# Kernel optimization log

Hardware: AMD Instinct MI355X
Metric: run time of the kernel (lower is better)

The kernel has to match this reference:

```python
import jax, jax.numpy as jnp
import numpy as np

NUM_HEADS = 16
KEY_DIM = 64
EPS = 1e-6


def setup_inputs() -> dict:
    key = jax.random.key(0)
    k0, k1, k2, k3, k4 = jax.random.split(key, 5)
    B, S, E = 4, 4096, NUM_HEADS * KEY_DIM
    scale = 1.0 / np.sqrt(KEY_DIM)
    return {
        "query": jax.random.normal(k0, (B, S, E), dtype=jnp.float32),
        "Wq": jax.random.normal(k1, (NUM_HEADS, KEY_DIM, KEY_DIM), dtype=jnp.float32) * scale,
        "Wk": jax.random.normal(k2, (NUM_HEADS, KEY_DIM, KEY_DIM), dtype=jnp.float32) * scale,
        "Wv": jax.random.normal(k3, (NUM_HEADS, KEY_DIM, KEY_DIM), dtype=jnp.float32) * scale,
        "Wo": jax.random.normal(k4, (E, E), dtype=jnp.float32) * (1.0 / np.sqrt(E)),
    }


def reference(query, Wq, Wk, Wv, Wo):
    # Self-attention: key = value = query (per call() defaults).
    B, S, E = query.shape
    H, D = NUM_HEADS, KEY_DIM
    # split_heads: (B, S, E) -> (B, H, S, D)
    x = jnp.transpose(query.reshape(B, S, H, D), (0, 2, 1, 3))
    # Per-head linear projections (all heads batched in one einsum each).
    q = jnp.einsum("bhsd,hde->bhse", x, Wq)
    k = jnp.einsum("bhsd,hde->bhse", x, Wk)
    v = jnp.einsum("bhsd,hde->bhse", x, Wv)
    # Kernel feature map phi(x) = elu(x) + 1 (strictly positive).
    phi_q = jax.nn.elu(q) + 1.0
    phi_k = jax.nn.elu(k) + 1.0
    # Linear (non-causal) attention: O(S*D^2) instead of O(S^2*D).
    kv = jnp.einsum("bhsd,bhse->bhde", phi_k, v)        # (B,H,D,D)
    k_sum = jnp.sum(phi_k, axis=2)                       # (B,H,D)
    z = jnp.einsum("bhsd,bhd->bhs", phi_q, k_sum)        # (B,H,S)
    ctx = jnp.einsum("bhsd,bhde->bhse", phi_q, kv) / (z[..., None] + EPS)
    # combine_heads: (B,H,S,D) -> (B,S,E), then output projection (no bias).
    combined = jnp.transpose(ctx, (0, 2, 1, 3)).reshape(B, S, H * D)
    return combined @ Wo
```

## Files before the change

### kernel.cpp

```cpp
#include <hip/hip_runtime.h>
#include <stdint.h>

#define S_LEN 4096
#define NHEADS 16
#define DHEAD 64
#define EMB 1024
#define NBATCH 4
#define NBH (NBATCH * NHEADS)

typedef unsigned short u16t;
typedef __attribute__((ext_vector_type(8))) short short8;
typedef __attribute__((ext_vector_type(4))) float f32x4;

__device__ __forceinline__ u16t f2bf(float f) {
  unsigned int x = __float_as_uint(f);
  x += 0x7fffu + ((x >> 16) & 1u);
  return (u16t)(x >> 16);
}
__device__ __forceinline__ unsigned int pack2(float a, float b) {
  return (unsigned int)f2bf(a) | ((unsigned int)f2bf(b) << 16);
}
__device__ __forceinline__ float bf2f(u16t u) { return __uint_as_float(((unsigned int)u) << 16); }
__device__ __forceinline__ float phifn(float v) { return v > 0.f ? v + 1.f : __expf(v); }

__device__ __forceinline__ void stage_x_bf16(const float* __restrict__ xg,
                                             u16t* __restrict__ xs, int t) {
#pragma unroll
  for (int i = 0; i < 8; ++i) {
    int fi = i * 256 + t;
    int r = fi >> 4, c4 = fi & 15;
    float4 v = *(const float4*)(xg + (size_t)r * EMB + c4 * 4);
    uint2 p;
    p.x = pack2(v.x, v.y);
    p.y = pack2(v.z, v.w);
    *(uint2*)(&xs[r * 72 + c4 * 4]) = p;
  }
}

__device__ __forceinline__ void stage_w8k(const u16t* __restrict__ wg,
                                          u16t* __restrict__ lds, int t) {
#pragma unroll
  for (int c = 0; c < 2; ++c) {
    const u16t* src = wg + (size_t)(c * 256 + t) * 8;
    char* dst = (char*)lds + c * 4096 + ((t >> 6) << 10);
    __builtin_amdgcn_global_load_lds((const __attribute__((address_space(1))) unsigned int*)src,
                                     (__attribute__((address_space(3))) unsigned int*)dst,
                                     16, 0, 0);
  }
}

__global__ __launch_bounds__(256) void la_prep(const float* __restrict__ Wq,
                                               const float* __restrict__ Wk,
                                               const float* __restrict__ Wv,
                                               u16t* __restrict__ WqT,
                                               u16t* __restrict__ WkT,
                                               u16t* __restrict__ WvT) {
  __shared__ float tmp[64][65];
  int blk = blockIdx.x;
  int mat = blk >> 4, h = blk & 15;
  const float* src = (mat == 0 ? Wq : (mat == 1 ? Wk : Wv)) + (size_t)h * 4096;
  u16t* dst = (mat == 0 ? WqT : (mat == 1 ? WkT : WvT)) + (size_t)h * 4096;
  int t = threadIdx.x;
#pragma unroll
  for (int p = 0; p < 16; ++p) {
    int i = p * 256 + t;
    tmp[i >> 6][i & 63] = src[i];
  }
  __syncthreads();
#pragma unroll
  for (int p = 0; p < 16; ++p) {
    int i = p * 256 + t;
    int e = i >> 6, r = i & 63, o = r >> 3, j = r & 7;
    dst[i] = f2bf(tmp[((o ^ (e & 7)) << 3) + j][e]);
  }
}

__global__ __launch_bounds__(256) void la_wot(const float* __restrict__ Wo,
                                              u16t* __restrict__ WoT) {
  __shared__ float t[64][65];
  int n0 = blockIdx.x * 64, k0 = blockIdx.y * 64;
  int tx = threadIdx.x, ty = threadIdx.y;
  for (int r = ty; r < 64; r += 4) t[r][tx] = Wo[(size_t)(k0 + r) * EMB + n0 + tx];
  __syncthreads();
  for (int r = ty; r < 64; r += 4)
    WoT[(size_t)(n0 + r) * EMB + k0 + tx] = f2bf(t[tx][r]);
}

__global__ __launch_bounds__(256) void la_kv2(const float* __restrict__ q,
                                              const u16t* __restrict__ WkT,
                                              const u16t* __restrict__ WvT,
                                              float* __restrict__ kvpart,
                                              float* __restrict__ kspart) {
  union Sm {
    struct { u16t xs[128 * 72]; u16t wk[4096]; u16t wv[4096]; } a;
    struct { u16t pkT[64 * 136]; u16t vT[64 * 136]; } b;
  };
  __shared__ Sm sm;
  int blk = blockIdx.x;
  int bh = blk >> 5, tile = blk & 31;
  int b = bh >> 4, h = bh & 15;
  int s0 = tile << 7;
  int t = threadIdx.x;
  int wave = t >> 6, lane = t & 63, l16 = lane & 15, g = lane >> 4;

  stage_x_bf16(q + ((size_t)b * S_LEN + s0) * EMB + h * 64, sm.a.xs, t);
  stage_w8k(WkT + (size_t)h * 4096, sm.a.wk, t);
  stage_w8k(WvT + (size_t)h * 4096, sm.a.wv, t);
  __syncthreads();

  f32x4 aK[2][4], aV[2][4];
#pragma unroll
  for (int m = 0; m < 2; ++m)
#pragma unroll
    for (int n = 0; n < 4; ++n) { aK[m][n] = 0.f; aV[m][n] = 0.f; }

  short8 af[2][2];
#pragma unroll
  for (int m = 0; m < 2; ++m)
#pragma unroll
    for (int kk = 0; kk < 2; ++kk)
      af[m][kk] = *(const short8*)(&sm.a.xs[(wave * 32 + m * 16 + l16) * 72 + kk * 32 + g * 8]);
#pragma unroll
  for (int n = 0; n < 4; ++n) {
    int e = n * 16 + l16;
#pragma unroll
    for (int kk = 0; kk < 2; ++kk) {
      int op = (kk * 4 + g) ^ (l16 & 7);
      short8 bK = *(const short8*)(&sm.a.wk[e * 64 + op * 8]);
      short8 bV = *(const short8*)(&sm.a.wv[e * 64 + op * 8]);
#pragma unroll
      for (int m = 0; m < 2; ++m) {
        aK[m][n] = __builtin_amdgcn_mfma_f32_16x16x32_bf16(af[m][kk], bK, aK[m][n], 0, 0, 0);
        aV[m][n] = __builtin_amdgcn_mfma_f32_16x16x32_bf16(af[m][kk], bV, aV[m][n], 0, 0, 0);
      }
    }
  }
  __syncthreads();

#pragma unroll
  for (int m = 0; m < 2; ++m)
#pragma unroll
    for (int n = 0; n < 4; ++n) {
      int e = n * 16 + l16;
#pragma unroll
      for (int j = 0; j < 4; ++j) {
        int s = wave * 32 + m * 16 + g * 4 + j;
        sm.b.pkT[e * 136 + s] = f2bf(phifn(aK[m][n][j]));
        sm.b.vT[e * 136 + s] = f2bf(aV[m][n][j]);
      }
    }
  __syncthreads();

  f32x4 kacc[4];
#pragma unroll
  for (int n = 0; n < 4; ++n) kacc[n] = 0.f;
#pragma unroll
  for (int ks = 0; ks < 4; ++ks) {
    short8 pa = *(const short8*)(&sm.b.pkT[(wave * 16 + l16) * 136 + ks * 32 + g * 8]);
#pragma unroll
    for (int n = 0; n < 4; ++n) {
      short8 vb = *(const short8*)(&sm.b.vT[(n * 16 + l16) * 136 + ks * 32 + g * 8]);
      kacc[n] = __builtin_amdgcn_mfma_f32_16x16x32_bf16(pa, vb, kacc[n], 0, 0, 0);
    }
  }
  float* kp = kvpart + (size_t)blk * 4096;
#pragma unroll
  for (int n = 0; n < 4; ++n)
#pragma unroll
    for (int j = 0; j < 4; ++j)
      kp[(wave * 16 + g * 4 + j) * 64 + n * 16 + l16] = kacc[n][j];

  if (t < 64) {
    float a = 0.f;
#pragma unroll 8
    for (int s = 0; s < 128; ++s) a += bf2f(sm.b.pkT[t * 136 + s]);
    kspart[(size_t)blk * 64 + t] = a;
  }
}

__global__ __launch_bounds__(256) void la_red2(const float* __restrict__ kvpart,
                                               const float* __restrict__ kspart,
                                               u16t* __restrict__ kvT_g,
                                               float* __restrict__ ksum_g) {
  __shared__ float kvs[64][65];
  int bh = blockIdx.x, t = threadIdx.x;
  float acc[16];
#pragma unroll
  for (int p = 0; p < 16; ++p) acc[p] = 0.f;
  for (int part = 0; part < 32; ++part) {
    const float* base = kvpart + ((size_t)bh * 32 + part) * 4096;
#pragma unroll
    for (int p = 0; p < 16; ++p) acc[p] += base[p * 256 + t];
  }
#pragma unroll
  for (int p = 0; p < 16; ++p) {
    int i = p * 256 + t;
    kvs[i >> 6][i & 63] = acc[p];
  }
  if (t < 64) {
    float a = 0.f;
    for (int part = 0; part < 32; ++part) a += kspart[((size_t)bh * 32 + part) * 64 + t];
    ksum_g[(size_t)bh * 64 + t] = a;
  }
  __syncthreads();
#pragma unroll
  for (int p = 0; p < 16; ++p) {
    int i = p * 256 + t;
    int e = i >> 6, r = i & 63, o = r >> 3, j = r & 7;
    kvT_g[(size_t)bh * 4096 + i] = f2bf(kvs[((o ^ (e & 7)) << 3) + j][e]);
  }
}

__global__ __launch_bounds__(256) void la_ctx2(const float* __restrict__ q,
                                               const u16t* __restrict__ WqT,
                                               const u16t* __restrict__ kvT_g,
                                               const float* __restrict__ ksum_g,
                                               u16t* __restrict__ comb) {
  __shared__ u16t xs[128 * 72];
  __shared__ u16t wq[4096];
  __shared__ u16t kvt[4096];
  __shared__ float ks[64];
  int blk = blockIdx.x;
  int bh = blk >> 5, tile = blk & 31;
  int b = bh >> 4, h = bh & 15;
  int s0 = tile << 7;
  int t = threadIdx.x;
  int wave = t >> 6, lane = t & 63, l16 = lane & 15, g = lane >> 4;

  stage_x_bf16(q + ((size_t)b * S_LEN + s0) * EMB + h * 64, xs, t);
  stage_w8k(WqT + (size_t)h * 4096, wq, t);
  stage_w8k(kvT_g + (size_t)bh * 4096, kvt, t);
  if (t < 64) ks[t] = ksum_g[(size_t)bh * 64 + t];
  __syncthreads();

  f32x4 aQ[2][4];
#pragma unroll
  for (int m = 0; m < 2; ++m)
#pragma unroll
    for (int n = 0; n < 4; ++n) aQ[m][n] = 0.f;
  short8 af[2][2];
#pragma unroll
  for (int m = 0; m < 2; ++m)
#pragma unroll
    for (int kk = 0; kk < 2; ++kk)
      af[m][kk] = *(const short8*)(&xs[(wave * 32 + m * 16 + l16) * 72 + kk * 32 + g * 8]);
#pragma unroll
  for (int n = 0; n < 4; ++n) {
    int e = n * 16 + l16;
#pragma unroll
    for (int kk = 0; kk < 2; ++kk) {
      int op = (kk * 4 + g) ^ (l16 & 7);
      short8 bQ = *(const short8*)(&wq[e * 64 + op * 8]);
#pragma unroll
      for (int m = 0; m < 2; ++m)
        aQ[m][n] = __builtin_amdgcn_mfma_f32_16x16x32_bf16(af[m][kk], bQ, aQ[m][n], 0, 0, 0);
    }
  }

  float ph[2][4][4];
#pragma unroll
  for (int m = 0; m < 2; ++m)
#pragma unroll
    for (int n = 0; n < 4; ++n)
#pragma unroll
      for (int j = 0; j < 4; ++j) ph[m][n][j] = phifn(aQ[m][n][j]);

  float z[2][4];
#pragma unroll
  for (int m = 0; m < 2; ++m)
#pragma unroll
    for (int j = 0; j < 4; ++j) {
      float zp = 0.f;
#pragma unroll
      for (int n = 0; n < 4; ++n) zp = fmaf(ph[m][n][j], ks[n * 16 + l16], zp);
      zp += __shfl_xor(zp, 1);
      zp += __shfl_xor(zp, 2);
      zp += __shfl_xor(zp, 4);
      zp += __shfl_xor(zp, 8);
      z[m][j] = zp;
    }
  __syncthreads();

#pragma unroll
  for (int m = 0; m < 2; ++m)
#pragma unroll
    for (int n = 0; n < 4; ++n)
#pragma unroll
      for (int j = 0; j < 4; ++j)
        xs[(wave * 32 + m * 16 + g * 4 + j) * 72 + n * 16 + l16] = f2bf(ph[m][n][j]);
  __syncthreads();

  f32x4 nacc[2][4];
#pragma unroll
  for (int m = 0; m < 2; ++m)
#pragma unroll
    for (int n = 0; n < 4; ++n) nacc[m][n] = 0.f;
#pragma unroll
  for (int kk = 0; kk < 2; ++kk) {
    short8 pa[2];
#pragma unroll
    for (int m = 0; m < 2; ++m)
      pa[m] = *(const short8*)(&xs[(wave * 32 + m * 16 + l16) * 72 + kk * 32 + g * 8]);
#pragma unroll
    for (int n = 0; n < 4; ++n) {
      int e = n * 16 + l16;
      int op = (kk * 4 + g) ^ (l16 & 7);
      short8 kb = *(const short8*)(&kvt[e * 64 + op * 8]);
#pragma unroll
      for (int m = 0; m < 2; ++m)
        nacc[m][n] = __builtin_amdgcn_mfma_f32_16x16x32_bf16(pa[m], kb, nacc[m][n], 0, 0, 0);
    }
  }
  __syncthreads();

#pragma unroll
  for (int m = 0; m < 2; ++m)
#pragma unroll
    for (int j = 0; j < 4; ++j) {
      float inv = 1.f / (z[m][j] + 1e-6f);
      int s = wave * 32 + m * 16 + g * 4 + j;
#pragma unroll
      for (int n = 0; n < 4; ++n)
        xs[s * 72 + n * 16 + l16] = f2bf(nacc[m][n][j] * inv);
    }
  __syncthreads();

#pragma unroll
  for (int i = 0; i < 4; ++i) {
    int c = i * 256 + t;
    int r = c >> 3, qd = c & 7;
    uint4 v = *(const uint4*)(&xs[r * 72 + qd * 8]);
    *(uint4*)(&comb[((size_t)b * S_LEN + s0 + r) * EMB + h * 64 + qd * 8]) = v;
  }
}

__device__ __forceinline__ void stage_half(const u16t* __restrict__ gbase,
                                           u16t* __restrict__ lbuf,
                                           int half, int t) {
#pragma unroll
  for (int it = 0; it < 2; ++it) {
    int slot = it * 512 + t;
    int row = half * 128 + (slot >> 3);
    int oct = slot & 7;
    const u16t* src = gbase + (size_t)row * EMB + (((oct ^ (row & 7)) << 3));
    char* dst = (char*)lbuf + ((half * 128 + it * 64 + ((t >> 6) << 3)) << 7);
    __builtin_amdgcn_global_load_lds((const __attribute__((address_space(1))) unsigned int*)src,
                                     (__attribute__((address_space(3))) unsigned int*)dst,
                                     16, 0, 0);
  }
}

#define GFENCE asm volatile("" ::: "memory")

#define PHASE(QM, QN, STAGE_STMT, WAIT_STMT)                                              \
  do {                                                                                    \
    short8 paf[4][2], pbf[2][2];                                                          \
    _Pragma("unroll") for (int mi = 0; mi < 4; ++mi) _Pragma("unroll")                    \
        for (int kk = 0; kk < 2; ++kk) {                                                  \
      int rr = (QM) * 128 + wr2 * 64 + mi * 16 + l16;                                     \
      paf[mi][kk] = *(const short8*)((const char*)Acur + rr * 128 +                       \
                                     ((((kk << 2) | g) ^ (rr & 7)) << 4));                \
    }                                                                                     \
    _Pragma("unroll") for (int ni = 0; ni < 2; ++ni) _Pragma("unroll")                    \
        for (int kk = 0; kk < 2; ++kk) {                                                  \
      int rr = (QN) * 128 + wc2 * 32 + ni * 16 + l16;                                     \
      pbf[ni][kk] = *(const short8*)((const char*)Bcur + rr * 128 +                       \
                                     ((((kk << 2) | g) ^ (rr & 7)) << 4));                \
    }                                                                                     \
    STAGE_STMT;                                                                           \
    WAIT_STMT;                                                                            \
    __builtin_amdgcn_s_barrier();                                                         \
    GFENCE;                                                                               \
    __builtin_amdgcn_s_setprio(1);                                                        \
    _Pragma("unroll") for (int mi = 0; mi < 4; ++mi) _Pragma("unroll")                    \
        for (int ni = 0; ni < 2; ++ni) {                                                  \
      acc[QM][QN][mi][ni] = __builtin_amdgcn_mfma_f32_16x16x32_bf16(                      \
          paf[mi][0], pbf[ni][0], acc[QM][QN][mi][ni], 0, 0, 0);                          \
      acc[QM][QN][mi][ni] = __builtin_amdgcn_mfma_f32_16x16x32_bf16(                      \
          paf[mi][1], pbf[ni][1], acc[QM][QN][mi][ni], 0, 0, 0);                          \
    }                                                                                     \
    __builtin_amdgcn_s_setprio(0);                                                        \
    GFENCE;                                                                               \
    __builtin_amdgcn_s_barrier();                                                         \
    GFENCE;                                                                               \
  } while (0)

__global__ __launch_bounds__(512, 2) void la_gemm8(const u16t* __restrict__ A,
                                                   const u16t* __restrict__ Bt,
                                                   float* __restrict__ C) {
  __shared__ u16t Al[2][16384];
  __shared__ u16t Bl[2][16384];
  int t = threadIdx.x;
  int bid = blockIdx.x;
  int swz = ((bid & 7) << 5) + (bid >> 3);
  int mt = swz >> 2, nt = swz & 3;
  const int M0 = mt * 256, N0 = nt * 256;
  int wave = t >> 6, lane = t & 63;
  int l16 = lane & 15, g = lane >> 4;
  int wr2 = wave >> 2, wc2 = wave & 3;

  f32x4 acc[2][2][4][2];
#pragma unroll
  for (int qm = 0; qm < 2; ++qm)
#pragma unroll
    for (int qn = 0; qn < 2; ++qn)
#pragma unroll
      for (int mi = 0; mi < 4; ++mi)
#pragma unroll
        for (int ni = 0; ni < 2; ++ni) acc[qm][qn][mi][ni] = 0.f;

  const u16t* Asrc = A + (size_t)M0 * EMB;
  const u16t* Bsrc = Bt + (size_t)N0 * EMB;

  stage_half(Asrc, Al[0], 0, t);
  stage_half(Bsrc, Bl[0], 0, t);
  stage_half(Bsrc, Bl[0], 1, t);
  stage_half(Asrc, Al[0], 1, t);
  asm volatile("s_waitcnt vmcnt(4)" ::: "memory");
  __builtin_amdgcn_s_barrier();
  GFENCE;

  for (int kt = 0; kt < 15; ++kt) {
    const u16t* Acur = Al[kt & 1];
    const u16t* Bcur = Bl[kt & 1];
    u16t* Anxt = Al[(kt + 1) & 1];
    u16t* Bnxt = Bl[(kt + 1) & 1];
    const u16t* An = Asrc + (kt + 1) * 64;
    const u16t* Bn = Bsrc + (kt + 1) * 64;
    PHASE(0, 0, { stage_half(An, Anxt, 0, t); stage_half(Bn, Bnxt, 0, t); },
          asm volatile("s_waitcnt vmcnt(6)" ::: "memory"));
    PHASE(0, 1, { stage_half(Bn, Bnxt, 1, t); },
          asm volatile("s_waitcnt vmcnt(6)" ::: "memory"));
    PHASE(1, 0, { stage_half(An, Anxt, 1, t); }, GFENCE);
    PHASE(1, 1, {}, asm volatile("s_waitcnt vmcnt(4)" ::: "memory"));
  }
  {
    const u16t* Acur = Al[1];
    const u16t* Bcur = Bl[1];
    PHASE(0, 0, {}, asm volatile("s_waitcnt vmcnt(2)" ::: "memory"));
    PHASE(0, 1, {}, asm volatile("s_waitcnt vmcnt(0)" ::: "memory"));
    PHASE(1, 0, {}, GFENCE);
    PHASE(1, 1, {}, GFENCE);
  }

#pragma unroll
  for (int qm = 0; qm < 2; ++qm)
#pragma unroll
    for (int qn = 0; qn < 2; ++qn)
#pragma unroll
      for (int mi = 0; mi < 4; ++mi)
#pragma unroll
        for (int ni = 0; ni < 2; ++ni)
#pragma unroll
          for (int j = 0; j < 4; ++j) {
            int row = M0 + qm * 128 + wr2 * 64 + mi * 16 + g * 4 + j;
            int col = N0 + qn * 128 + wc2 * 32 + ni * 16 + l16;
            C[(size_t)row * EMB + col] = acc[qm][qn][mi][ni][j];
          }
}

extern "C" void kernel_launch(void* const* d_in, const int* in_sizes, int n_in,
                              void* d_out, int out_size, void* d_ws, size_t ws_size,
                              hipStream_t stream) {
  const float* query = (const float*)d_in[0];
  const float* Wq = (const float*)d_in[1];
  const float* Wk = (const float*)d_in[2];
  const float* Wv = (const float*)d_in[3];
  const float* Wo = (const float*)d_in[4];
  float* out = (float*)d_out;
  char* ws = (char*)d_ws;

  u16t* WoT     = (u16t*)(ws);
  u16t* WqT     = (u16t*)(ws + 2097152);
  u16t* WkT     = (u16t*)(ws + 2228224);
  u16t* WvT     = (u16t*)(ws + 2359296);
  float* kvpart = (float*)(ws + 2490368);
  float* kspart = (float*)(ws + 36044800);
  u16t* kvT_g   = (u16t*)(ws + 36569088);
  float* ksum_g = (float*)(ws + 37093376);
  u16t* comb    = (u16t*)(ws + 37109760);

  la_prep<<<48, 256, 0, stream>>>(Wq, Wk, Wv, WqT, WkT, WvT);
  la_wot<<<dim3(16, 16), dim3(64, 4), 0, stream>>>(Wo, WoT);
  la_kv2<<<NBH * 32, 256, 0, stream>>>(query, WkT, WvT, kvpart, kspart);
  la_red2<<<NBH, 256, 0, stream>>>(kvpart, kspart, kvT_g, ksum_g);
  la_ctx2<<<NBH * 32, 256, 0, stream>>>(query, WqT, kvT_g, ksum_g, comb);
  la_gemm8<<<256, 512, 0, stream>>>(comb, WoT, out);
}
```

Baseline: 122.7 us.

## Fold per-head kv into output projection and compute phi(q) in single query pass

The kv and ctx kernels are merged, so each block reads its query slice once, computes Q, K and V projections together, writes bf16 phi(q), and accumulates partial kv over four 128-row chunks with fewer partial blocks. The reduction kernel now multiplies each head's kv matrix into the matching slice of Wo, giving a per-batch fused weight, so the final GEMM multiplies normalized phi(q) directly and the separate ctx matmul goes away. A small kernel applies the 1/z normalization, and the GEMM's load/MFMA phase order is reshuffled to reuse B fragments across quadrants. This adds an extra phi(q) round trip through memory and per-batch weight matrices, plus extra bf16 rounding of kv·Wo.

```diff
diff --git a/kernel.cpp b/kernel.cpp
--- a/kernel.cpp
+++ b/kernel.cpp
@@ -86,251 +86,228 @@
     WoT[(size_t)(n0 + r) * EMB + k0 + tx] = f2bf(t[tx][r]);
 }
 
-__global__ __launch_bounds__(256) void la_kv2(const float* __restrict__ q,
-                                              const u16t* __restrict__ WkT,
-                                              const u16t* __restrict__ WvT,
-                                              float* __restrict__ kvpart,
-                                              float* __restrict__ kspart) {
-  union Sm {
-    struct { u16t xs[128 * 72]; u16t wk[4096]; u16t wv[4096]; } a;
-    struct { u16t pkT[64 * 136]; u16t vT[64 * 136]; } b;
-  };
-  __shared__ Sm sm;
+__global__ __launch_bounds__(256) void la_kvq3(const float* __restrict__ q,
+                                               const u16t* __restrict__ WqT,
+                                               const u16t* __restrict__ WkT,
+                                               const u16t* __restrict__ WvT,
+                                               u16t* __restrict__ phiq,
+                                               float* __restrict__ kvpart,
+                                               float* __restrict__ kspart) {
+  __shared__ u16t xs[128 * 72];
+  __shared__ u16t wq[4096];
+  __shared__ u16t wk[4096];
+  __shared__ u16t wv[4096];
+  __shared__ u16t pkT[64 * 136];
+  __shared__ u16t vT[64 * 136];
   int blk = blockIdx.x;
-  int bh = blk >> 5, tile = blk & 31;
+  int bh = blk >> 3, tile = blk & 7;
   int b = bh >> 4, h = bh & 15;
-  int s0 = tile << 7;
+  int s0 = tile << 9;
   int t = threadIdx.x;
   int wave = t >> 6, lane = t & 63, l16 = lane & 15, g = lane >> 4;
 
-  stage_x_bf16(q + ((size_t)b * S_LEN + s0) * EMB + h * 64, sm.a.xs, t);
-  stage_w8k(WkT + (size_t)h * 4096, sm.a.wk, t);
-  stage_w8k(WvT + (size_t)h * 4096, sm.a.wv, t);
-  __syncthreads();
-
-  f32x4 aK[2][4], aV[2][4];
-#pragma unroll
-  for (int m = 0; m < 2; ++m)
-#pragma unroll
-    for (int n = 0; n < 4; ++n) { aK[m][n] = 0.f; aV[m][n] = 0.f; }
-
-  short8 af[2][2];
-#pragma unroll
-  for (int m = 0; m < 2; ++m)
-#pragma unroll
-    for (int kk = 0; kk < 2; ++kk)
-      af[m][kk] = *(const short8*)(&sm.a.xs[(wave * 32 + m * 16 + l16) * 72 + kk * 32 + g * 8]);
-#pragma unroll
-  for (int n = 0; n < 4; ++n) {
-    int e = n * 16 + l16;
-#pragma unroll
-    for (int kk = 0; kk < 2; ++kk) {
-      int op = (kk * 4 + g) ^ (l16 & 7);
-      short8 bK = *(const short8*)(&sm.a.wk[e * 64 + op * 8]);
-      short8 bV = *(const short8*)(&sm.a.wv[e * 64 + op * 8]);
-#pragma unroll
-      for (int m = 0; m < 2; ++m) {
-        aK[m][n] = __builtin_amdgcn_mfma_f32_16x16x32_bf16(af[m][kk], bK, aK[m][n], 0, 0, 0);
-        aV[m][n] = __builtin_amdgcn_mfma_f32_16x16x32_bf16(af[m][kk], bV, aV[m][n], 0, 0, 0);
-      }
-    }
-  }
-  __syncthreads();
-
-#pragma unroll
-  for (int m = 0; m < 2; ++m)
+  stage_w8k(WqT + (size_t)h * 4096, wq, t);
+  stage_w8k(WkT + (size_t)h * 4096, wk, t);
+  stage_w8k(WvT + (size_t)h * 4096, wv, t);
+
+  f32x4 kacc[4];
+#pragma unroll
+  for (int n = 0; n < 4; ++n) kacc[n] = 0.f;
+  float ksacc = 0.f;
+
+  for (int c = 0; c < 4; ++c) {
+    if (c) __syncthreads();
+    stage_x_bf16(q + ((size_t)b * S_LEN + s0 + c * 128) * EMB + h * 64, xs, t);
+    __syncthreads();
+
+    f32x4 aQ[2][4], aK[2][4], aV[2][4];
+#pragma unroll
+    for (int m = 0; m < 2; ++m)
+#pragma unroll
+      for (int n = 0; n < 4; ++n) { aQ[m][n] = 0.f; aK[m][n] = 0.f; aV[m][n] = 0.f; }
+    short8 af[2][2];
+#pragma unroll
+    for (int m = 0; m < 2; ++m)
+#pragma unroll
+      for (int kk = 0; kk < 2; ++kk)
+        af[m][kk] = *(const short8*)(&xs[(wave * 32 + m * 16 + l16) * 72 + kk * 32 + g * 8]);
 #pragma unroll
     for (int n = 0; n < 4; ++n) {
       int e = n * 16 + l16;
 #pragma unroll
-      for (int j = 0; j < 4; ++j) {
-        int s = wave * 32 + m * 16 + g * 4 + j;
-        sm.b.pkT[e * 136 + s] = f2bf(phifn(aK[m][n][j]));
-        sm.b.vT[e * 136 + s] = f2bf(aV[m][n][j]);
+      for (int kk = 0; kk < 2; ++kk) {
+        int op = (kk * 4 + g) ^ (l16 & 7);
+        short8 bQ = *(const short8*)(&wq[e * 64 + op * 8]);
+        short8 bK = *(const short8*)(&wk[e * 64 + op * 8]);
+        short8 bV = *(const short8*)(&wv[e * 64 + op * 8]);
+#pragma unroll
+        for (int m = 0; m < 2; ++m) {
+          aQ[m][n] = __builtin_amdgcn_mfma_f32_16x16x32_bf16(af[m][kk], bQ, aQ[m][n], 0, 0, 0);
+          aK[m][n] = __builtin_amdgcn_mfma_f32_16x16x32_bf16(af[m][kk], bK, aK[m][n], 0, 0, 0);
+          aV[m][n] = __builtin_amdgcn_mfma_f32_16x16x32_bf16(af[m][kk], bV, aV[m][n], 0, 0, 0);
+        }
       }
     }
-  __syncthreads();
-
-  f32x4 kacc[4];
-#pragma unroll
-  for (int n = 0; n < 4; ++n) kacc[n] = 0.f;
-#pragma unroll
-  for (int ks = 0; ks < 4; ++ks) {
-    short8 pa = *(const short8*)(&sm.b.pkT[(wave * 16 + l16) * 136 + ks * 32 + g * 8]);
-#pragma unroll
-    for (int n = 0; n < 4; ++n) {
-      short8 vb = *(const short8*)(&sm.b.vT[(n * 16 + l16) * 136 + ks * 32 + g * 8]);
-      kacc[n] = __builtin_amdgcn_mfma_f32_16x16x32_bf16(pa, vb, kacc[n], 0, 0, 0);
-    }
-  }
+    __syncthreads();
+
+#pragma unroll
+    for (int m = 0; m < 2; ++m)
+#pragma unroll
+      for (int n = 0; n < 4; ++n) {
+        int e = n * 16 + l16;
+#pragma unroll
+        for (int j = 0; j < 4; ++j) {
+          int s = wave * 32 + m * 16 + g * 4 + j;
+          xs[s * 72 + e] = f2bf(phifn(aQ[m][n][j]));
+          pkT[e * 136 + s] = f2bf(phifn(aK[m][n][j]));
+          vT[e * 136 + s] = f2bf(aV[m][n][j]);
+        }
+      }
+    __syncthreads();
+
+#pragma unroll
+    for (int i = 0; i < 4; ++i) {
+      int slot = i * 256 + t;
+      int r = slot >> 3, cc = (slot & 7) * 8;
+      *(uint4*)(phiq + ((size_t)bh * S_LEN + s0 + c * 128 + r) * 64 + cc) =
+          *(const uint4*)(&xs[r * 72 + cc]);
+    }
+#pragma unroll
+    for (int ks = 0; ks < 4; ++ks) {
+      short8 pa = *(const short8*)(&pkT[(wave * 16 + l16) * 136 + ks * 32 + g * 8]);
+#pragma unroll
+      for (int n = 0; n < 4; ++n) {
+        short8 vb = *(const short8*)(&vT[(n * 16 + l16) * 136 + ks * 32 + g * 8]);
+        kacc[n] = __builtin_amdgcn_mfma_f32_16x16x32_bf16(pa, vb, kacc[n], 0, 0, 0);
+      }
+    }
+    if (t < 64) {
+#pragma unroll 8
+      for (int s = 0; s < 128; ++s) ksacc += bf2f(pkT[t * 136 + s]);
+    }
+  }
+
   float* kp = kvpart + (size_t)blk * 4096;
 #pragma unroll
   for (int n = 0; n < 4; ++n)
 #pragma unroll
     for (int j = 0; j < 4; ++j)
       kp[(wave * 16 + g * 4 + j) * 64 + n * 16 + l16] = kacc[n][j];
-
+  if (t < 64) kspart[(size_t)blk * 64 + t] = ksacc;
+}
+
+__global__ __launch_bounds__(256) void la_red3(const float* __restrict__ kvpart,
+                                               const float* __restrict__ kspart,
+                                               const u16t* __restrict__ WoT,
+                                               float* __restrict__ ksum_g,
+                                               u16t* __restrict__ W2T) {
+  __shared__ float kvs[64][65];
+  __shared__ u16t aT[256 * 72];
+  int bh = blockIdx.x;
+  int b = bh >> 4, h = bh & 15;
+  int t = threadIdx.x, wave = t >> 6, lane = t & 63, l16 = lane & 15, g = lane >> 4;
+
+  float acc[16];
+#pragma unroll
+  for (int i = 0; i < 16; ++i) acc[i] = 0.f;
+  for (int p = 0; p < 8; ++p) {
+    const float* base = kvpart + ((size_t)bh * 8 + p) * 4096;
+#pragma unroll
+    for (int i = 0; i < 16; ++i) acc[i] += base[i * 256 + t];
+  }
+#pragma unroll
+  for (int i = 0; i < 16; ++i) {
+    int idx = i * 256 + t;
+    kvs[idx >> 6][idx & 63] = acc[i];
+  }
   if (t < 64) {
     float a = 0.f;
-#pragma unroll 8
-    for (int s = 0; s < 128; ++s) a += bf2f(sm.b.pkT[t * 136 + s]);
-    kspart[(size_t)blk * 64 + t] = a;
-  }
-}
-
-__global__ __launch_bounds__(256) void la_red2(const float* __restrict__ kvpart,
-                                               const float* __restrict__ kspart,
-                                               u16t* __restrict__ kvT_g,
-                                               float* __restrict__ ksum_g) {
-  __shared__ float kvs[64][65];
-  int bh = blockIdx.x, t = threadIdx.x;
-  float acc[16];
-#pragma unroll
-  for (int p = 0; p < 16; ++p) acc[p] = 0.f;
-  for (int part = 0; part < 32; ++part) {
-    const float* base = kvpart + ((size_t)bh * 32 + part) * 4096;
-#pragma unroll
-    for (int p = 0; p < 16; ++p) acc[p] += base[p * 256 + t];
-  }
-#pragma unroll
-  for (int p = 0; p < 16; ++p) {
-    int i = p * 256 + t;
-    kvs[i >> 6][i & 63] = acc[p];
-  }
-  if (t < 64) {
-    float a = 0.f;
-    for (int part = 0; part < 32; ++part) a += kspart[((size_t)bh * 32 + part) * 64 + t];
+    for (int p = 0; p < 8; ++p) a += kspart[((size_t)bh * 8 + p) * 64 + t];
     ksum_g[(size_t)bh * 64 + t] = a;
   }
   __syncthreads();
-#pragma unroll
-  for (int p = 0; p < 16; ++p) {
-    int i = p * 256 + t;
-    int e = i >> 6, r = i & 63, o = r >> 3, j = r & 7;
-    kvT_g[(size_t)bh * 4096 + i] = f2bf(kvs[((o ^ (e & 7)) << 3) + j][e]);
-  }
-}
-
-__global__ __launch_bounds__(256) void la_ctx2(const float* __restrict__ q,
-                                               const u16t* __restrict__ WqT,
-                                               const u16t* __restrict__ kvT_g,
-                                               const float* __restrict__ ksum_g,
-                                               u16t* __restrict__ comb) {
-  __shared__ u16t xs[128 * 72];
-  __shared__ u16t wq[4096];
-  __shared__ u16t kvt[4096];
+
+  short8 kvbf[4][2];
+#pragma unroll
+  for (int n = 0; n < 4; ++n)
+#pragma unroll
+    for (int kk = 0; kk < 2; ++kk) {
+      u16t* pp = (u16t*)&kvbf[n][kk];
+#pragma unroll
+      for (int i = 0; i < 8; ++i) pp[i] = f2bf(kvs[n * 16 + l16][kk * 32 + g * 8 + i]);
+    }
+
+  for (int ec = 0; ec < 4; ++ec) {
+    if (ec) __syncthreads();
+#pragma unroll
+    for (int p = 0; p < 8; ++p) {
+      int slot = p * 256 + t;
+      int r = slot >> 3, cc = (slot & 7) * 8;
+      *(uint4*)(&aT[r * 72 + cc]) =
+          *(const uint4*)(WoT + (size_t)(ec * 256 + r) * 1024 + h * 64 + cc);
+    }
+    __syncthreads();
+    f32x4 c2[4][4];
+#pragma unroll
+    for (int mi = 0; mi < 4; ++mi)
+#pragma unroll
+      for (int n = 0; n < 4; ++n) c2[mi][n] = 0.f;
+#pragma unroll
+    for (int kk = 0; kk < 2; ++kk)
+#pragma unroll
+      for (int mi = 0; mi < 4; ++mi) {
+        short8 afr = *(const short8*)(&aT[(wave * 64 + mi * 16 + l16) * 72 + kk * 32 + g * 8]);
+#pragma unroll
+        for (int n = 0; n < 4; ++n)
+          c2[mi][n] = __builtin_amdgcn_mfma_f32_16x16x32_bf16(afr, kvbf[n][kk], c2[mi][n], 0, 0, 0);
+      }
+    __syncthreads();
+#pragma unroll
+    for (int mi = 0; mi < 4; ++mi)
+#pragma unroll
+      for (int n = 0; n < 4; ++n)
+#pragma unroll
+        for (int j = 0; j < 4; ++j)
+          aT[(wave * 64 + mi * 16 + g * 4 + j) * 72 + n * 16 + l16] = f2bf(c2[mi][n][j]);
+    __syncthreads();
+#pragma unroll
+    for (int p = 0; p < 8; ++p) {
+      int slot = p * 256 + t;
+      int r = slot >> 3, cc = (slot & 7) * 8;
+      *(uint4*)(W2T + ((size_t)b << 20) + (size_t)(ec * 256 + r) * 1024 + h * 64 + cc) =
+          *(const uint4*)(&aT[r * 72 + cc]);
+    }
+  }
+}
+
+__global__ __launch_bounds__(256) void la_scale(const u16t* __restrict__ phiq,
+                                                const float* __restrict__ ksum_g,
+                                                u16t* __restrict__ phiq2) {
   __shared__ float ks[64];
   int blk = blockIdx.x;
-  int bh = blk >> 5, tile = blk & 31;
+  int bh = blk >> 4, sl = blk & 15;
   int b = bh >> 4, h = bh & 15;
-  int s0 = tile << 7;
+  int s0 = sl * 256;
   int t = threadIdx.x;
-  int wave = t >> 6, lane = t & 63, l16 = lane & 15, g = lane >> 4;
-
-  stage_x_bf16(q + ((size_t)b * S_LEN + s0) * EMB + h * 64, xs, t);
-  stage_w8k(WqT + (size_t)h * 4096, wq, t);
-  stage_w8k(kvT_g + (size_t)bh * 4096, kvt, t);
   if (t < 64) ks[t] = ksum_g[(size_t)bh * 64 + t];
   __syncthreads();
-
-  f32x4 aQ[2][4];
-#pragma unroll
-  for (int m = 0; m < 2; ++m)
-#pragma unroll
-    for (int n = 0; n < 4; ++n) aQ[m][n] = 0.f;
-  short8 af[2][2];
-#pragma unroll
-  for (int m = 0; m < 2; ++m)
-#pragma unroll
-    for (int kk = 0; kk < 2; ++kk)
-      af[m][kk] = *(const short8*)(&xs[(wave * 32 + m * 16 + l16) * 72 + kk * 32 + g * 8]);
-#pragma unroll
-  for (int n = 0; n < 4; ++n) {
-    int e = n * 16 + l16;
-#pragma unroll
-    for (int kk = 0; kk < 2; ++kk) {
-      int op = (kk * 4 + g) ^ (l16 & 7);
-      short8 bQ = *(const short8*)(&wq[e * 64 + op * 8]);
-#pragma unroll
-      for (int m = 0; m < 2; ++m)
-        aQ[m][n] = __builtin_amdgcn_mfma_f32_16x16x32_bf16(af[m][kk], bQ, aQ[m][n], 0, 0, 0);
-    }
-  }
-
-  float ph[2][4][4];
-#pragma unroll
-  for (int m = 0; m < 2; ++m)
-#pragma unroll
-    for (int n = 0; n < 4; ++n)
-#pragma unroll
-      for (int j = 0; j < 4; ++j) ph[m][n][j] = phifn(aQ[m][n][j]);
-
-  float z[2][4];
-#pragma unroll
-  for (int m = 0; m < 2; ++m)
-#pragma unroll
-    for (int j = 0; j < 4; ++j) {
-      float zp = 0.f;
-#pragma unroll
-      for (int n = 0; n < 4; ++n) zp = fmaf(ph[m][n][j], ks[n * 16 + l16], zp);
-      zp += __shfl_xor(zp, 1);
-      zp += __shfl_xor(zp, 2);
-      zp += __shfl_xor(zp, 4);
-      zp += __shfl_xor(zp, 8);
-      z[m][j] = zp;
-    }
-  __syncthreads();
-
-#pragma unroll
-  for (int m = 0; m < 2; ++m)
-#pragma unroll
-    for (int n = 0; n < 4; ++n)
-#pragma unroll
-      for (int j = 0; j < 4; ++j)
-        xs[(wave * 32 + m * 16 + g * 4 + j) * 72 + n * 16 + l16] = f2bf(ph[m][n][j]);
-  __syncthreads();
-
-  f32x4 nacc[2][4];
-#pragma unroll
-  for (int m = 0; m < 2; ++m)
-#pragma unroll
-    for (int n = 0; n < 4; ++n) nacc[m][n] = 0.f;
-#pragma unroll
-  for (int kk = 0; kk < 2; ++kk) {
-    short8 pa[2];
-#pragma unroll
-    for (int m = 0; m < 2; ++m)
-      pa[m] = *(const short8*)(&xs[(wave * 32 + m * 16 + l16) * 72 + kk * 32 + g * 8]);
-#pragma unroll
-    for (int n = 0; n < 4; ++n) {
-      int e = n * 16 + l16;
-      int op = (kk * 4 + g) ^ (l16 & 7);
-      short8 kb = *(const short8*)(&kvt[e * 64 + op * 8]);
-#pragma unroll
-      for (int m = 0; m < 2; ++m)
-        nacc[m][n] = __builtin_amdgcn_mfma_f32_16x16x32_bf16(pa[m], kb, nacc[m][n], 0, 0, 0);
-    }
-  }
-  __syncthreads();
-
-#pragma unroll
-  for (int m = 0; m < 2; ++m)
-#pragma unroll
-    for (int j = 0; j < 4; ++j) {
-      float inv = 1.f / (z[m][j] + 1e-6f);
-      int s = wave * 32 + m * 16 + g * 4 + j;
-#pragma unroll
-      for (int n = 0; n < 4; ++n)
-        xs[s * 72 + n * 16 + l16] = f2bf(nacc[m][n][j] * inv);
-    }
-  __syncthreads();
-
-#pragma unroll
-  for (int i = 0; i < 4; ++i) {
-    int c = i * 256 + t;
-    int r = c >> 3, qd = c & 7;
-    uint4 v = *(const uint4*)(&xs[r * 72 + qd * 8]);
-    *(uint4*)(&comb[((size_t)b * S_LEN + s0 + r) * EMB + h * 64 + qd * 8]) = v;
+  int c16 = t & 15, rg = t >> 4;
+#pragma unroll 2
+  for (int it = 0; it < 16; ++it) {
+    int s = s0 + it * 16 + rg;
+    uint2 u = *(const uint2*)(phiq + ((size_t)bh * S_LEN + s) * 64 + c16 * 4);
+    float f0 = bf2f((u16t)(u.x & 0xffff)), f1 = bf2f((u16t)(u.x >> 16));
+    float f2 = bf2f((u16t)(u.y & 0xffff)), f3 = bf2f((u16t)(u.y >> 16));
+    float zp = f0 * ks[c16 * 4] + f1 * ks[c16 * 4 + 1] + f2 * ks[c16 * 4 + 2] + f3 * ks[c16 * 4 + 3];
+    zp += __shfl_xor(zp, 1);
+    zp += __shfl_xor(zp, 2);
+    zp += __shfl_xor(zp, 4);
+    zp += __shfl_xor(zp, 8);
+    float inv = 1.f / (zp + 1e-6f);
+    uint2 o;
+    o.x = pack2(f0 * inv, f1 * inv);
+    o.y = pack2(f2 * inv, f3 * inv);
+    *(uint2*)(phiq2 + ((size_t)(b * S_LEN + s)) * EMB + h * 64 + c16 * 4) = o;
   }
 }
 
@@ -352,41 +329,37 @@
 
 #define GFENCE asm volatile("" ::: "memory")
 
-#define PHASE(QM, QN, STAGE_STMT, WAIT_STMT)                                              \
-  do {                                                                                    \
-    short8 paf[4][2], pbf[2][2];                                                          \
-    _Pragma("unroll") for (int mi = 0; mi < 4; ++mi) _Pragma("unroll")                    \
-        for (int kk = 0; kk < 2; ++kk) {                                                  \
-      int rr = (QM) * 128 + wr2 * 64 + mi * 16 + l16;                                     \
-      paf[mi][kk] = *(const short8*)((const char*)Acur + rr * 128 +                       \
-                                     ((((kk << 2) | g) ^ (rr & 7)) << 4));                \
-    }                                                                                     \
-    _Pragma("unroll") for (int ni = 0; ni < 2; ++ni) _Pragma("unroll")                    \
-        for (int kk = 0; kk < 2; ++kk) {                                                  \
-      int rr = (QN) * 128 + wc2 * 32 + ni * 16 + l16;                                     \
-      pbf[ni][kk] = *(const short8*)((const char*)Bcur + rr * 128 +                       \
-                                     ((((kk << 2) | g) ^ (rr & 7)) << 4));                \
-    }                                                                                     \
-    STAGE_STMT;                                                                           \
-    WAIT_STMT;                                                                            \
-    __builtin_amdgcn_s_barrier();                                                         \
-    GFENCE;                                                                               \
-    __builtin_amdgcn_s_setprio(1);                                                        \
-    _Pragma("unroll") for (int mi = 0; mi < 4; ++mi) _Pragma("unroll")                    \
-        for (int ni = 0; ni < 2; ++ni) {                                                  \
-      acc[QM][QN][mi][ni] = __builtin_amdgcn_mfma_f32_16x16x32_bf16(                      \
-          paf[mi][0], pbf[ni][0], acc[QM][QN][mi][ni], 0, 0, 0);                          \
-      acc[QM][QN][mi][ni] = __builtin_amdgcn_mfma_f32_16x16x32_bf16(                      \
-          paf[mi][1], pbf[ni][1], acc[QM][QN][mi][ni], 0, 0, 0);                          \
-    }                                                                                     \
-    __builtin_amdgcn_s_setprio(0);                                                        \
-    GFENCE;                                                                               \
-    __builtin_amdgcn_s_barrier();                                                         \
-    GFENCE;                                                                               \
-  } while (0)
-
-__global__ __launch_bounds__(512, 2) void la_gemm8(const u16t* __restrict__ A,
-                                                   const u16t* __restrict__ Bt,
+#define LOAD_A(QM)                                                              \
+  _Pragma("unroll") for (int mi = 0; mi < 4; ++mi) _Pragma("unroll")            \
+      for (int kk = 0; kk < 2; ++kk) {                                          \
+    int rr = (QM) * 128 + wr2 * 64 + mi * 16 + l16;                             \
+    afr[mi][kk] = *(const short8*)((const char*)Acur + rr * 128 +               \
+                                   ((((kk << 2) | g) ^ (rr & 7)) << 4));        \
+  }
+#define LOAD_B(QN, DST)                                                         \
+  _Pragma("unroll") for (int ni = 0; ni < 2; ++ni) _Pragma("unroll")            \
+      for (int kk = 0; kk < 2; ++kk) {                                          \
+    int rr = (QN) * 128 + wc2 * 32 + ni * 16 + l16;                             \
+    DST[ni][kk] = *(const short8*)((const char*)Bcur + rr * 128 +               \
+                                   ((((kk << 2) | g) ^ (rr & 7)) << 4));        \
+  }
+#define MFMA_Q(QM, QN, BF)                                                      \
+  __builtin_amdgcn_s_setprio(1);                                                \
+  _Pragma("unroll") for (int mi = 0; mi < 4; ++mi) _Pragma("unroll")            \
+      for (int ni = 0; ni < 2; ++ni) {                                          \
+    acc[QM][QN][mi][ni] = __builtin_amdgcn_mfma_f32_16x16x32_bf16(              \
+        afr[mi][0], BF[ni][0], acc[QM][QN][mi][ni], 0, 0, 0);                   \
+    acc[QM][QN][mi][ni] = __builtin_amdgcn_mfma_f32_16x16x32_bf16(              \
+        afr[mi][1], BF[ni][1], acc[QM][QN][mi][ni], 0, 0, 0);                   \
+  }                                                                             \
+  __builtin_amdgcn_s_setprio(0);
+
+#define BAR()                      \
+  __builtin_amdgcn_s_barrier();    \
+  GFENCE
+
+__global__ __launch_bounds__(512, 2) void la_gemm9(const u16t* __restrict__ A,
+                                                   const u16t* __restrict__ W2T,
                                                    float* __restrict__ C) {
   __shared__ u16t Al[2][16384];
   __shared__ u16t Bl[2][16384];
@@ -395,6 +368,7 @@
   int swz = ((bid & 7) << 5) + (bid >> 3);
   int mt = swz >> 2, nt = swz & 3;
   const int M0 = mt * 256, N0 = nt * 256;
+  const int b = mt >> 4;
   int wave = t >> 6, lane = t & 63;
   int l16 = lane & 15, g = lane >> 4;
   int wr2 = wave >> 2, wc2 = wave & 3;
@@ -410,15 +384,16 @@
         for (int ni = 0; ni < 2; ++ni) acc[qm][qn][mi][ni] = 0.f;
 
   const u16t* Asrc = A + (size_t)M0 * EMB;
-  const u16t* Bsrc = Bt + (size_t)N0 * EMB;
+  const u16t* Bsrc = W2T + ((size_t)b << 20) + (size_t)N0 * EMB;
 
   stage_half(Asrc, Al[0], 0, t);
   stage_half(Bsrc, Bl[0], 0, t);
   stage_half(Bsrc, Bl[0], 1, t);
   stage_half(Asrc, Al[0], 1, t);
   asm volatile("s_waitcnt vmcnt(4)" ::: "memory");
-  __builtin_amdgcn_s_barrier();
-  GFENCE;
+  BAR();
+
+  short8 afr[4][2], bf0[2][2], bf1[2][2];
 
   for (int kt = 0; kt < 15; ++kt) {
     const u16t* Acur = Al[kt & 1];
@@ -427,20 +402,58 @@
     u16t* Bnxt = Bl[(kt + 1) & 1];
     const u16t* An = Asrc + (kt + 1) * 64;
     const u16t* Bn = Bsrc + (kt + 1) * 64;
-    PHASE(0, 0, { stage_half(An, Anxt, 0, t); stage_half(Bn, Bnxt, 0, t); },
-          asm volatile("s_waitcnt vmcnt(6)" ::: "memory"));
-    PHASE(0, 1, { stage_half(Bn, Bnxt, 1, t); },
-          asm volatile("s_waitcnt vmcnt(6)" ::: "memory"));
-    PHASE(1, 0, { stage_half(An, Anxt, 1, t); }, GFENCE);
-    PHASE(1, 1, {}, asm volatile("s_waitcnt vmcnt(4)" ::: "memory"));
+    LOAD_A(0);
+    LOAD_B(0, bf0);
+    stage_half(An, Anxt, 0, t);
+    stage_half(Bn, Bnxt, 0, t);
+    asm volatile("s_waitcnt vmcnt(6)" ::: "memory");
+    BAR();
+    MFMA_Q(0, 0, bf0);
+    GFENCE;
+    BAR();
+    LOAD_B(1, bf1);
+    stage_half(Bn, Bnxt, 1, t);
+    asm volatile("s_waitcnt vmcnt(6)" ::: "memory");
+    BAR();
+    MFMA_Q(0, 1, bf1);
+    GFENCE;
+    BAR();
+    LOAD_A(1);
+    stage_half(An, Anxt, 1, t);
+    BAR();
+    MFMA_Q(1, 1, bf1);
+    GFENCE;
+    BAR();
+    asm volatile("s_waitcnt vmcnt(4)" ::: "memory");
+    BAR();
+    MFMA_Q(1, 0, bf0);
+    GFENCE;
+    BAR();
   }
   {
     const u16t* Acur = Al[1];
     const u16t* Bcur = Bl[1];
-    PHASE(0, 0, {}, asm volatile("s_waitcnt vmcnt(2)" ::: "memory"));
-    PHASE(0, 1, {}, asm volatile("s_waitcnt vmcnt(0)" ::: "memory"));
-    PHASE(1, 0, {}, GFENCE);
-    PHASE(1, 1, {}, GFENCE);
+    LOAD_A(0);
+    LOAD_B(0, bf0);
+    asm volatile("s_waitcnt vmcnt(2)" ::: "memory");
+    BAR();
+    MFMA_Q(0, 0, bf0);
+    GFENCE;
+    BAR();
+    LOAD_B(1, bf1);
+    asm volatile("s_waitcnt vmcnt(0)" ::: "memory");
+    BAR();
+    MFMA_Q(0, 1, bf1);
+    GFENCE;
+    BAR();
+    LOAD_A(1);
+    BAR();
+    MFMA_Q(1, 1, bf1);
+    GFENCE;
+    BAR();
+    BAR();
+    MFMA_Q(1, 0, bf0);
+    GFENCE;
   }
 
 #pragma unroll
@@ -474,16 +487,17 @@
   u16t* WqT     = (u16t*)(ws + 2097152);
   u16t* WkT     = (u16t*)(ws + 2228224);
   u16t* WvT     = (u16t*)(ws + 2359296);
-  float* kvpart = (float*)(ws + 2490368);
-  float* kspart = (float*)(ws + 36044800);
-  u16t* kvT_g   = (u16t*)(ws + 36569088);
-  float* ksum_g = (float*)(ws + 37093376);
-  u16t* comb    = (u16t*)(ws + 37109760);
+  u16t* phiq    = (u16t*)(ws + 2490368);
+  float* kvpart = (float*)(ws + 36044800);
+  float* kspart = (float*)(ws + 44433408);
+  float* ksum_g = (float*)(ws + 44564480);
+  u16t* W2T     = (u16t*)(ws + 44580864);
+  u16t* phiq2   = (u16t*)(ws + 52969472);
 
   la_prep<<<48, 256, 0, stream>>>(Wq, Wk, Wv, WqT, WkT, WvT);
   la_wot<<<dim3(16, 16), dim3(64, 4), 0, stream>>>(Wo, WoT);
-  la_kv2<<<NBH * 32, 256, 0, stream>>>(query, WkT, WvT, kvpart, kspart);
-  la_red2<<<NBH, 256, 0, stream>>>(kvpart, kspart, kvT_g, ksum_g);
-  la_ctx2<<<NBH * 32, 256, 0, stream>>>(query, WqT, kvT_g, ksum_g, comb);
-  la_gemm8<<<256, 512, 0, stream>>>(comb, WoT, out);
-}
+  la_kvq3<<<512, 256, 0, stream>>>(query, WqT, WkT, WvT, phiq, kvpart, kspart);
+  la_red3<<<NBH, 256, 0, stream>>>(kvpart, kspart, WoT, ksum_g, W2T);
+  la_scale<<<1024, 256, 0, stream>>>(phiq, ksum_g, phiq2);
+  la_gemm9<<<256, 512, 0, stream>>>(phiq2, W2T, out);
+}
```

After: 114.8 us. 6.4% less time.
